# Optimization experiments

Measured on AMD Instinct MI355X. Metric: run time of the kernel, lower is better.

## Reference

```python
import jax, jax.numpy as jnp
import numpy as np

N = 50000
NEIGH = 32
D_IN = 128
D_OUT = 128

def setup_inputs() -> dict:
    key = jax.random.key(0)
    k1, k2, k3, k4 = jax.random.split(key, 4)
    self_vecs = jax.random.normal(k1, (N, D_IN), dtype=jnp.float32)
    neigh_vecs = jax.random.normal(k2, (N * NEIGH, D_IN), dtype=jnp.float32)
    weight = jax.random.normal(k3, (D_IN, D_OUT), dtype=jnp.float32) * (1.0 / np.sqrt(D_IN))
    bias = jax.random.normal(k4, (D_OUT,), dtype=jnp.float32) * 0.01
    return {"self_vecs": self_vecs, "neigh_vecs": neigh_vecs, "neigh_num": NEIGH,
            "weight": weight, "bias": bias}

def reference(self_vecs, neigh_vecs, neigh_num, weight, bias):
    # self_h: [N, 1, F], neigh_h: [N, neigh_num, F]
    self_h = jnp.matmul(self_vecs, weight)[:, None, :]
    neigh_h = jnp.matmul(neigh_vecs, weight).reshape(-1, neigh_num, weight.shape[1])
    # concat along neighbor axis then mean == mean of (neigh_num+1) rows
    out = jnp.mean(jnp.concatenate([self_h, neigh_h], axis=1), axis=1)
    return out + bias
```

## Files before the change

### kernel.cpp

```cpp
#include <hip/hip_runtime.h>


typedef float f32x4 __attribute__((ext_vector_type(4)));

constexpr int D       = 128;
constexpr int D4      = D / 4;
constexpr int NEIGH   = 32;
constexpr int WAVES   = 8;
constexpr int THREADS = WAVES * 64;
constexpr int NPW     = 4;
constexpr int NPB     = WAVES * NPW;

__global__ __launch_bounds__(THREADS, 4)
void sparse_layer_v3(const float* __restrict__ self_vecs,
                     const float* __restrict__ neigh_vecs,
                     const float* __restrict__ weight,
                     const float* __restrict__ bias,
                     float* __restrict__ out, int n_nodes)
{
    __shared__ float w_lds[D * D];
    __shared__ float agg_lds[WAVES][D];

    {
        const f32x4* w4 = reinterpret_cast<const f32x4*>(weight);
        f32x4*       wp = reinterpret_cast<f32x4*>(w_lds);
        #pragma unroll
        for (int i = 0; i < (D * D / 4) / THREADS; ++i)
            wp[threadIdx.x + i * THREADS] = w4[threadIdx.x + i * THREADS];
    }
    __syncthreads();

    const int wave = threadIdx.x >> 6;
    const int lane = threadIdx.x & 63;
    const int h    = lane >> 5;
    const int c4   = lane & 31;

    const f32x4* s4 = reinterpret_cast<const f32x4*>(self_vecs);
    const f32x4* g4 = reinterpret_cast<const f32x4*>(neigh_vecs);
    const f32x4* wl = reinterpret_cast<const f32x4*>(w_lds);
    f32x4* arow = reinterpret_cast<f32x4*>(agg_lds[wave]);
    const f32x4 bv = reinterpret_cast<const f32x4*>(bias)[c4];
    constexpr float inv = 1.0f / (NEIGH + 1);

    const long base = (long)blockIdx.x * NPB + wave * NPW;

    for (int i = 0; i < NPW; ++i) {
        const long n = base + i;
        if (n >= n_nodes) break;

        const f32x4* p = g4 + n * (long)NEIGH * D4;
        f32x4 acc = (f32x4)0.0f;
        if (h == 0) acc = s4[n * D4 + c4];
        #pragma unroll
        for (int l = 0; l < 16; ++l)
            acc += p[l * 64 + lane];

        f32x4 tot;
        tot.x = acc.x + __shfl_xor(acc.x, 32);
        tot.y = acc.y + __shfl_xor(acc.y, 32);
        tot.z = acc.z + __shfl_xor(acc.z, 32);
        tot.w = acc.w + __shfl_xor(acc.w, 32);
        tot *= inv;
        if (h == 0) arow[c4] = tot;

        f32x4 o = (f32x4)0.0f;
        #pragma unroll
        for (int k4 = 0; k4 < D4 / 2; ++k4) {
            const int kk = h * (D4 / 2) + k4;
            f32x4 a  = arow[kk];
            f32x4 w0 = wl[(4 * kk + 0) * D4 + c4];
            f32x4 w1 = wl[(4 * kk + 1) * D4 + c4];
            f32x4 w2 = wl[(4 * kk + 2) * D4 + c4];
            f32x4 w3 = wl[(4 * kk + 3) * D4 + c4];
            o += a.x * w0;  o += a.y * w1;  o += a.z * w2;  o += a.w * w3;
        }
        o.x += __shfl_xor(o.x, 32);
        o.y += __shfl_xor(o.y, 32);
        o.z += __shfl_xor(o.z, 32);
        o.w += __shfl_xor(o.w, 32);
        if (h == 0)
            reinterpret_cast<f32x4*>(out)[n * D4 + c4] = o + bv;
    }
}

extern "C" void kernel_launch(void* const* d_in, const int* in_sizes, int n_in,
                              void* d_out, int out_size, void* d_ws, size_t ws_size,
                              hipStream_t stream) {
    const float* self_vecs  = (const float*)d_in[0];
    const float* neigh_vecs = (const float*)d_in[1];
    const float* weight     = (const float*)d_in[3];
    const float* bias       = (const float*)d_in[4];
    float*       out        = (float*)d_out;

    const int n_nodes = in_sizes[0] / D;
    const int blocks  = (n_nodes + NPB - 1) / NPB;
    hipLaunchKernelGGL(sparse_layer_v3, dim3(blocks), dim3(THREADS), 0, stream,
                       self_vecs, neigh_vecs, weight, bias, out, n_nodes);
}
```

Before: 178.6 us.

## Drop LDS weight staging, batch four nodes per wave, use nontemporal streaming

Removes the 64KB LDS copy of the weight matrix. Weights are now read straight from global memory and reused across a batch of four nodes per wave in the matmul stage. Blocks shrink to four waves with a higher launch-bounds occupancy hint, so more waves can be resident to hide latency on the bandwidth-bound neighbour-sum stream. Neighbour and self reads and the output writes use nontemporal hints to avoid polluting the cache. The trade-off is that each wave now fetches weight tiles through L1/L2 instead of LDS, which adds cache traffic that competes with the main stream.

```diff
diff --git a/kernel.cpp b/kernel.cpp
--- a/kernel.cpp
+++ b/kernel.cpp
@@ -6,29 +6,19 @@
 constexpr int D       = 128;
 constexpr int D4      = D / 4;
 constexpr int NEIGH   = 32;
-constexpr int WAVES   = 8;
+constexpr int WAVES   = 4;
 constexpr int THREADS = WAVES * 64;
 constexpr int NPW     = 4;
 constexpr int NPB     = WAVES * NPW;
 
-__global__ __launch_bounds__(THREADS, 4)
-void sparse_layer_v3(const float* __restrict__ self_vecs,
+__global__ __launch_bounds__(THREADS, 6)
+void sparse_layer_v4(const float* __restrict__ self_vecs,
                      const float* __restrict__ neigh_vecs,
                      const float* __restrict__ weight,
                      const float* __restrict__ bias,
                      float* __restrict__ out, int n_nodes)
 {
-    __shared__ float w_lds[D * D];
-    __shared__ float agg_lds[WAVES][D];
-
-    {
-        const f32x4* w4 = reinterpret_cast<const f32x4*>(weight);
-        f32x4*       wp = reinterpret_cast<f32x4*>(w_lds);
-        #pragma unroll
-        for (int i = 0; i < (D * D / 4) / THREADS; ++i)
-            wp[threadIdx.x + i * THREADS] = w4[threadIdx.x + i * THREADS];
-    }
-    __syncthreads();
+    __shared__ float agg_lds[WAVES][NPW][D];
 
     const int wave = threadIdx.x >> 6;
     const int lane = threadIdx.x & 63;
@@ -37,49 +27,66 @@
 
     const f32x4* s4 = reinterpret_cast<const f32x4*>(self_vecs);
     const f32x4* g4 = reinterpret_cast<const f32x4*>(neigh_vecs);
-    const f32x4* wl = reinterpret_cast<const f32x4*>(w_lds);
-    f32x4* arow = reinterpret_cast<f32x4*>(agg_lds[wave]);
-    const f32x4 bv = reinterpret_cast<const f32x4*>(bias)[c4];
+    const f32x4* w4 = reinterpret_cast<const f32x4*>(weight);
     constexpr float inv = 1.0f / (NEIGH + 1);
 
     const long base = (long)blockIdx.x * NPB + wave * NPW;
 
+    #pragma unroll
     for (int i = 0; i < NPW; ++i) {
         const long n = base + i;
         if (n >= n_nodes) break;
-
         const f32x4* p = g4 + n * (long)NEIGH * D4;
         f32x4 acc = (f32x4)0.0f;
-        if (h == 0) acc = s4[n * D4 + c4];
-        #pragma unroll
+        if (h == 0) acc = __builtin_nontemporal_load(&s4[n * D4 + c4]);
+        #pragma unroll 8
         for (int l = 0; l < 16; ++l)
-            acc += p[l * 64 + lane];
-
+            acc += __builtin_nontemporal_load(&p[l * 64 + lane]);
         f32x4 tot;
         tot.x = acc.x + __shfl_xor(acc.x, 32);
         tot.y = acc.y + __shfl_xor(acc.y, 32);
         tot.z = acc.z + __shfl_xor(acc.z, 32);
         tot.w = acc.w + __shfl_xor(acc.w, 32);
-        tot *= inv;
-        if (h == 0) arow[c4] = tot;
+        if (h == 0)
+            reinterpret_cast<f32x4*>(agg_lds[wave][i])[c4] = tot * inv;
+    }
 
-        f32x4 o = (f32x4)0.0f;
-        #pragma unroll
-        for (int k4 = 0; k4 < D4 / 2; ++k4) {
-            const int kk = h * (D4 / 2) + k4;
-            f32x4 a  = arow[kk];
-            f32x4 w0 = wl[(4 * kk + 0) * D4 + c4];
-            f32x4 w1 = wl[(4 * kk + 1) * D4 + c4];
-            f32x4 w2 = wl[(4 * kk + 2) * D4 + c4];
-            f32x4 w3 = wl[(4 * kk + 3) * D4 + c4];
-            o += a.x * w0;  o += a.y * w1;  o += a.z * w2;  o += a.w * w3;
-        }
+    f32x4 o0 = (f32x4)0.0f, o1 = (f32x4)0.0f, o2 = (f32x4)0.0f, o3 = (f32x4)0.0f;
+    const f32x4* a0 = reinterpret_cast<const f32x4*>(agg_lds[wave][0]);
+    const f32x4* a1 = reinterpret_cast<const f32x4*>(agg_lds[wave][1]);
+    const f32x4* a2 = reinterpret_cast<const f32x4*>(agg_lds[wave][2]);
+    const f32x4* a3 = reinterpret_cast<const f32x4*>(agg_lds[wave][3]);
+
+    #pragma unroll 4
+    for (int k4 = 0; k4 < D4 / 2; ++k4) {
+        const int kk = h * (D4 / 2) + k4;
+        f32x4 w0 = w4[(4 * kk + 0) * D4 + c4];
+        f32x4 w1 = w4[(4 * kk + 1) * D4 + c4];
+        f32x4 w2 = w4[(4 * kk + 2) * D4 + c4];
+        f32x4 w3 = w4[(4 * kk + 3) * D4 + c4];
+        f32x4 b0 = a0[kk];
+        f32x4 b1 = a1[kk];
+        f32x4 b2 = a2[kk];
+        f32x4 b3 = a3[kk];
+        o0 += b0.x * w0;  o0 += b0.y * w1;  o0 += b0.z * w2;  o0 += b0.w * w3;
+        o1 += b1.x * w0;  o1 += b1.y * w1;  o1 += b1.z * w2;  o1 += b1.w * w3;
+        o2 += b2.x * w0;  o2 += b2.y * w1;  o2 += b2.z * w2;  o2 += b2.w * w3;
+        o3 += b3.x * w0;  o3 += b3.y * w1;  o3 += b3.z * w2;  o3 += b3.w * w3;
+    }
+
+    const f32x4 bv = reinterpret_cast<const f32x4*>(bias)[c4];
+    f32x4* o4 = reinterpret_cast<f32x4*>(out);
+    f32x4 oo[NPW] = {o0, o1, o2, o3};
+    #pragma unroll
+    for (int i = 0; i < NPW; ++i) {
+        f32x4 o = oo[i];
         o.x += __shfl_xor(o.x, 32);
         o.y += __shfl_xor(o.y, 32);
         o.z += __shfl_xor(o.z, 32);
         o.w += __shfl_xor(o.w, 32);
-        if (h == 0)
-            reinterpret_cast<f32x4*>(out)[n * D4 + c4] = o + bv;
+        const long n = base + i;
+        if (h == 0 && n < n_nodes)
+            __builtin_nontemporal_store(o + bv, &o4[n * D4 + c4]);
     }
 }
 
@@ -94,6 +101,6 @@
 
     const int n_nodes = in_sizes[0] / D;
     const int blocks  = (n_nodes + NPB - 1) / NPB;
-    hipLaunchKernelGGL(sparse_layer_v3, dim3(blocks), dim3(THREADS), 0, stream,
+    hipLaunchKernelGGL(sparse_layer_v4, dim3(blocks), dim3(THREADS), 0, stream,
                        self_vecs, neigh_vecs, weight, bias, out, n_nodes);
 }
```

Measured after the change: 160.2 us, median of 2. 1.11x faster.
